# Kernel tuning notes

Hardware: AMD Instinct MI355X
Metric: run time of the kernel (lower is better)

## Reference

```python
import jax, jax.numpy as jnp
import numpy as np

B, H, W, ENC = 64, 14, 14, 2048
A, E, D, V, T = 512, 512, 512, 10000, 21


def setup_inputs() -> dict:
    key = jax.random.key(0)
    ks = jax.random.split(key, 24)
    f = lambda k, shape, s: (jax.random.normal(k, shape, jnp.float32) * s)
    inp = {
        'encoder_out': f(ks[0], (B, H, W, ENC), 1.0),
        'encoded_captions': jax.random.randint(ks[1], (B, T), 0, V),
        'caption_lengths': jax.random.randint(ks[2], (B,), 0, T + 1),
        'emb': jax.random.uniform(ks[3], (V, E), jnp.float32, -0.1, 0.1),
        'enc_att_W': f(ks[4], (ENC, A), 0.02), 'enc_att_b': jnp.zeros((A,), jnp.float32),
        'dec_att_W': f(ks[5], (D, A), 0.04), 'dec_att_b': jnp.zeros((A,), jnp.float32),
        'full_att_W': f(ks[6], (A, 1), 0.04), 'full_att_b': jnp.zeros((1,), jnp.float32),
        'init_h_W': f(ks[7], (ENC, D), 0.02), 'init_h_b': jnp.zeros((D,), jnp.float32),
        'init_c_W': f(ks[8], (ENC, D), 0.02), 'init_c_b': jnp.zeros((D,), jnp.float32),
        'f_beta_W': f(ks[9], (D, ENC), 0.04), 'f_beta_b': jnp.zeros((ENC,), jnp.float32),
        'W_ih': f(ks[10], (4 * D, E + ENC), 0.02), 'b_ih': jnp.zeros((4 * D,), jnp.float32),
        'W_hh': f(ks[11], (4 * D, D), 0.04), 'b_hh': jnp.zeros((4 * D,), jnp.float32),
        'fc_W': jax.random.uniform(ks[12], (D, V), jnp.float32, -0.1, 0.1),
        'fc_b': jnp.zeros((V,), jnp.float32),
    }
    return inp


def reference(encoder_out, encoded_captions, caption_lengths, emb,
              enc_att_W, enc_att_b, dec_att_W, dec_att_b, full_att_W, full_att_b,
              init_h_W, init_h_b, init_c_W, init_c_b, f_beta_W, f_beta_b,
              W_ih, b_ih, W_hh, b_hh, fc_W, fc_b):
    b = encoder_out.shape[0]
    enc = encoder_out.reshape(b, -1, encoder_out.shape[-1])  # (B, P, ENC)
    cl = jnp.clip(caption_lengths.reshape(-1), 1, None)
    sort_ind = jnp.argsort(-cl)  # descending by length
    cl = cl[sort_ind]
    enc = enc[sort_ind]
    caps = encoded_captions[sort_ind]
    dec_len = cl - 1  # (B,)

    embs = emb[caps]  # (B, T, E)
    mean_enc = enc.mean(axis=1)
    h0 = jnp.tanh(mean_enc @ init_h_W + init_h_b)
    c0 = jnp.tanh(mean_enc @ init_c_W + init_c_b)

    att1 = enc @ enc_att_W + enc_att_b  # (B, P, A), loop-invariant
    Tdec = caps.shape[1] - 1
    embs_t = jnp.swapaxes(embs[:, :Tdec], 0, 1)  # (Tdec, B, E)

    def step(carry, xs):
        h, c = carry
        t, x_emb = xs
        active = (t < dec_len)[:, None]  # (B,1)
        att2 = h @ dec_att_W + dec_att_b  # (B, A)
        e = jnp.squeeze(jax.nn.relu(att1 + att2[:, None, :]) @ full_att_W, -1) + full_att_b[0]  # (B,P)
        alpha = jax.nn.softmax(e + 1e-8, axis=1)
        awe = jnp.einsum('bpe,bp->be', enc, alpha)  # (B, ENC)
        gate = jax.nn.sigmoid(h @ f_beta_W + f_beta_b)
        awe = gate * awe
        x = jnp.concatenate([x_emb, awe], axis=1)  # (B, E+ENC)
        gates = x @ W_ih.T + b_ih + h @ W_hh.T + b_hh  # (B, 4D)
        i, f, g, o = jnp.split(gates, 4, axis=1)
        c_new = jax.nn.sigmoid(f) * c + jax.nn.sigmoid(i) * jnp.tanh(g)
        h_new = jax.nn.sigmoid(o) * jnp.tanh(c_new)
        preds = h_new @ fc_W + fc_b
        h = jnp.where(active, h_new, h)
        c = jnp.where(active, c_new, c)
        preds = jnp.where(active, preds, 0.0)
        alpha = jnp.where(active, alpha, 0.0)
        return (h, c), (preds, alpha)

    (_, _), (preds, alphas) = jax.lax.scan(step, (h0, c0), (jnp.arange(Tdec), embs_t))
    predictions = jnp.swapaxes(preds, 0, 1)  # (B, Tdec, V)
    alphas = jnp.swapaxes(alphas, 0, 1)      # (B, Tdec, P)
    return predictions, caps, dec_len, alphas, sort_ind
```

## Files before the change

### kernel.cpp

```cpp
#include <hip/hip_runtime.h>
#include <cstddef>


namespace {

typedef _Float16 f16;
typedef f16 f16x8 __attribute__((ext_vector_type(8)));
typedef f16 f16x4 __attribute__((ext_vector_type(4)));
typedef f16 f16x2 __attribute__((ext_vector_type(2)));
typedef float f32x4 __attribute__((ext_vector_type(4)));

constexpr int NB = 64, NP = 196, NE = 2048, NA = 512, ND = 512, NV = 10000;
constexpr int NT_CAP = 21, NTD = 20;
constexpr int KC = 3072;
constexpr int LDT = 40;
constexpr int LDK = 72;

constexpr size_t OFF_ATT1   = 0;
constexpr size_t OFF_DAW    = 12845056;
constexpr size_t OFF_FBW    = 13369344;
constexpr size_t OFF_EAW    = 15466496;
constexpr size_t OFF_IHW    = 17563648;
constexpr size_t OFF_ICW    = 19660800;
constexpr size_t OFF_FCW    = 15466496;
constexpr size_t OFF_WCAT   = 25755648;
constexpr size_t OFF_MEAN16 = 38338560;
constexpr size_t OFF_H16    = 38600704;
constexpr size_t OFF_HNEW16 = 38666240;
constexpr size_t OFF_C      = 38731776;
constexpr size_t OFF_ATT2   = 38862848;
constexpr size_t OFF_GATE   = 38993920;
constexpr size_t OFF_ALPHA  = 39518208;
constexpr size_t OFF_XCAT   = 39569408;
constexpr size_t OFF_INT    = 39962624;
constexpr size_t OFF_BCAT   = 39970816;
constexpr size_t OFF_ENC16  = 39979008;
constexpr size_t FULL_BYTES = 91359232;
constexpr size_t OFF_HSEQ   = FULL_BYTES;
constexpr size_t FULL2_BYTES = FULL_BYTES + (size_t)NTD * NB * ND * 2;
constexpr size_t OFF_HWHH   = FULL2_BYTES;
constexpr size_t OFF_EMBW   = OFF_HWHH + 524288;
constexpr size_t OFF_EMBS   = OFF_EMBW + 10485760;
constexpr size_t FULL3_BYTES = OFF_EMBS + 1310720;

__device__ __forceinline__ float sigmoidf_(float x) { return 1.0f / (1.0f + expf(-x)); }

__device__ __forceinline__ void stage16(const f16* __restrict__ src, int lda, int k0,
                                        f16* __restrict__ lds, int tid) {
  const int row = tid >> 2, seg = tid & 3;
  *(f16x8*)&lds[row * LDT + seg * 8] =
      *(const f16x8*)&src[(size_t)row * lda + k0 + seg * 8];
}

__device__ __forceinline__ void cvt8(const float* __restrict__ p, f16* __restrict__ dst) {
  const float4 a = *(const float4*)p;
// ... 295 lines not shown
                                                 f16* __restrict__ att1) {
  __shared__ __align__(16) f16 lA[64 * LDK];
  __shared__ __align__(16) f16 lB[128 * LDK];
  const int r0 = blockIdx.x * 64, n0 = blockIdx.y * 128;
  const int tid = threadIdx.x, lane = tid & 63, wv = tid >> 6;
  const int col = lane & 15, quad = lane >> 4;
  const int wr = wv >> 1, wc = wv & 1;
  const int arow = tid >> 2, aseg = (tid & 3) * 16;
  const int brow = tid >> 1, bseg = (tid & 1) * 32;
  const f16* gA = enc16 + (size_t)(r0 + arow) * NE + aseg;
  const f16* gB = eaWt + (size_t)(n0 + brow) * NE + bseg;
  f16* wA = &lA[arow * LDK + aseg];
  f16* wB = &lB[brow * LDK + bseg];
  f32x4 acc[2][4] = {};
  for (int k0 = 0; k0 < NE; k0 += 64) {
    *(f16x8*)(wA)      = *(const f16x8*)(gA + k0);
    *(f16x8*)(wA + 8)  = *(const f16x8*)(gA + k0 + 8);
    *(f16x8*)(wB)      = *(const f16x8*)(gB + k0);
    *(f16x8*)(wB + 8)  = *(const f16x8*)(gB + k0 + 8);
    *(f16x8*)(wB + 16) = *(const f16x8*)(gB + k0 + 16);
    *(f16x8*)(wB + 24) = *(const f16x8*)(gB + k0 + 24);
    __syncthreads();
#pragma unroll
    for (int kh = 0; kh < 2; ++kh) {
      f16x8 a[2], b[4];
#pragma unroll
      for (int i = 0; i < 2; ++i)
        a[i] = *(const f16x8*)&lA[(wr * 32 + i * 16 + col) * LDK + kh * 32 + quad * 8];
#pragma unroll
      for (int j = 0; j < 4; ++j)
        b[j] = *(const f16x8*)&lB[(wc * 64 + j * 16 + col) * LDK + kh * 32 + quad * 8];
#pragma unroll
      for (int i = 0; i < 2; ++i)
#pragma unroll
        for (int j = 0; j < 4; ++j)
          acc[i][j] = __builtin_amdgcn_mfma_f32_16x16x32_f16(a[i], b[j], acc[i][j], 0, 0, 0);
    }
    __syncthreads();
  }
#pragma unroll
  for (int j = 0; j < 4; ++j) {
    const int n = n0 + wc * 64 + j * 16 + col;
    const float bv = eab[n];
#pragma unroll
    for (int i = 0; i < 2; ++i)
#pragma unroll
      for (int rr = 0; rr < 4; ++rr) {
        const int r = r0 + wr * 32 + i * 16 + quad * 4 + rr;
        att1[(size_t)r * NA + n] = (f16)(acc[i][j][rr] + bv);
      }
  }
}

__global__ __launch_bounds__(256) void k_hgemm_v2(const f16* __restrict__ h16,
                                                  const f16* __restrict__ daWt,
                                                  const float* __restrict__ dab,
                                                  const f16* __restrict__ fbWt,
                                                  const float* __restrict__ fbb,
                                                  float* __restrict__ att2,
                                                  float* __restrict__ gate) {
  __shared__ float R[2 * 64 * 16];
  const int tid = threadIdx.x, lane = tid & 63, wv = tid >> 6;
  const int col = lane & 15, quad = lane >> 4;
  const int sub = wv >> 1, kh = wv & 1;
  const int nt = blockIdx.x * 2 + sub;
  const bool is_att = nt < 32;
  const f16* Brow = is_att ? (daWt + (size_t)nt * 16 * ND)
                           : (fbWt + (size_t)(nt - 32) * 16 * ND);
  f32x4 acc[4] = {};
  wave_gemm64(h16, Brow, ND, kh * 256, kh * 256 + 256, col, quad, acc);
  if (kh) {
#pragma unroll
    for (int mt = 0; mt < 4; ++mt)
#pragma unroll
      for (int rr = 0; rr < 4; ++rr)
        R[(sub * 64 + lane) * 16 + mt * 4 + rr] = acc[mt][rr];
  }
  __syncthreads();
  if (kh) return;
#pragma unroll
  for (int mt = 0; mt < 4; ++mt)
#pragma unroll
    for (int rr = 0; rr < 4; ++rr)
      acc[mt][rr] += R[(sub * 64 + lane) * 16 + mt * 4 + rr];
  if (is_att) {
    const int n = nt * 16 + col;
#pragma unroll
    for (int mt = 0; mt < 4; ++mt)
#pragma unroll
      for (int rr = 0; rr < 4; ++rr) {
        const int m = mt * 16 + quad * 4 + rr;
        att2[(size_t)m * NA + n] = acc[mt][rr] + dab[n];
      }
  } else {
    const int n = (nt - 32) * 16 + col;
#pragma unroll
    for (int mt = 0; mt < 4; ++mt)
#pragma unroll
      for (int rr = 0; rr < 4; ++rr) {
        const int m = mt * 16 + quad * 4 + rr;
        gate[(size_t)m * NE + n] = sigmoidf_(acc[mt][rr] + fbb[n]);
      }
  }
}

__global__ __launch_bounds__(256) void k_hall(const f16* __restrict__ h16,
                                              const f16* __restrict__ daWt,
                                              const float* __restrict__ dab,
                                              const f16* __restrict__ fbWt,
                                              const float* __restrict__ fbb,
                                              const f16* __restrict__ Wcat2,
                                              float* __restrict__ att2,
                                              float* __restrict__ gate,
                                              float* __restrict__ hwhh) {
  __shared__ float R[4 * 1024];
  const int nt = blockIdx.x;
  const int tid = threadIdx.x, lane = tid & 63, wv = tid >> 6;
  const int col = lane & 15, quad = lane >> 4;
  const f16* Brow; int ldb;
  if (nt < 32)       { Brow = daWt + (size_t)nt * 16 * ND; ldb = ND; }
  else if (nt < 160) { Brow = fbWt + (size_t)(nt - 32) * 16 * ND; ldb = ND; }
  else               { Brow = Wcat2 + (size_t)(nt - 160) * 16 * KC + 2560; ldb = KC; }
  f32x4 acc[4] = {};
  wave_gemm_s<4>(h16, ND, Brow, ldb, wv * 128, wv * 128 + 128, col, quad, acc);
#pragma unroll
  for (int mt = 0; mt < 4; ++mt)
#pragma unroll
    for (int rr = 0; rr < 4; ++rr)
      R[wv * 1024 + (mt * 4 + rr) * 64 + lane] = acc[mt][rr];
  __syncthreads();
#pragma unroll
  for (int j = 0; j < 4; ++j) {
    const int slot = tid * 4 + j;
    const float s = R[slot] + R[1024 + slot] + R[2048 + slot] + R[3072 + slot];
    const int c2 = slot >> 6;
    const int lane_s = slot & 63;
    const int mt = c2 >> 2, rr = c2 & 3;
    const int m = mt * 16 + (lane_s >> 4) * 4 + rr;
    const int nl = lane_s & 15;
    if (nt < 32) {
      const int n = nt * 16 + nl;
      att2[(size_t)m * NA + n] = s + dab[n];
    } else if (nt < 160) {
      const int n = (nt - 32) * 16 + nl;
      gate[(size_t)m * NE + n] = sigmoidf_(s + fbb[n]);
    } else {
      const int r = (nt - 160) * 16 + nl;
      hwhh[(size_t)m * NE + r] = s;
    }
  }
}

__global__ __launch_bounds__(512) void k_logits(const f16* __restrict__ att1,
                                                const float* __restrict__ att2,
                                                const float* __restrict__ fullW,
                                                const int* __restrict__ declen, int t,
                                                float* __restrict__ alpha_ws,
                                                float* __restrict__ out_alphas) {
  const int b = blockIdx.x;
  const int tid = threadIdx.x, wv = tid >> 6, lane = tid & 63;
  __shared__ float e[200];
  __shared__ float red2[2];
  {
    float a2r[8], fwr[8];
    const float4* A2 = (const float4*)(att2 + (size_t)b * NA + lane * 8);
    const float4* FW = (const float4*)(fullW + lane * 8);
    const float4 q0 = A2[0], q1 = A2[1], w0 = FW[0], w1 = FW[1];
    a2r[0] = q0.x; a2r[1] = q0.y; a2r[2] = q0.z; a2r[3] = q0.w;
    a2r[4] = q1.x; a2r[5] = q1.y; a2r[6] = q1.z; a2r[7] = q1.w;
    fwr[0] = w0.x; fwr[1] = w0.y; fwr[2] = w0.z; fwr[3] = w0.w;
    fwr[4] = w1.x; fwr[5] = w1.y; fwr[6] = w1.z; fwr[7] = w1.w;
    for (int p = wv; p < NP; p += 8) {
      const f16x8 row = *(const f16x8*)(att1 + ((size_t)b * NP + p) * NA + lane * 8);
      float acc = 0.0f;
#pragma unroll
      for (int j = 0; j < 8; ++j) acc += fmaxf((float)row[j] + a2r[j], 0.0f) * fwr[j];
#pragma unroll
      for (int off = 32; off > 0; off >>= 1) acc += __shfl_down(acc, off, 64);
      if (lane == 0) e[p] = acc;
    }
  }
  __syncthreads();
  if (wv == 0) {
    const float v0 = e[lane];
    const float v1 = e[lane + 64];
    const float v2 = e[lane + 128];
    const float v3 = (lane < 4) ? e[192 + lane] : -INFINITY;
    float mx = fmaxf(fmaxf(v0, v1), fmaxf(v2, v3));
#pragma unroll
    for (int off = 32; off > 0; off >>= 1) mx = fmaxf(mx, __shfl_xor(mx, off, 64));
    float s = expf(v0 - mx) + expf(v1 - mx) + expf(v2 - mx) +
              ((lane < 4) ? expf(v3 - mx) : 0.0f);
#pragma unroll
    for (int off = 32; off > 0; off >>= 1) s += __shfl_xor(s, off, 64);
    if (lane == 0) { red2[0] = mx; red2[1] = 1.0f / s; }
  }
  __syncthreads();
  if (tid < NP) {
    const float a = expf(e[tid] - red2[0]) * red2[1];
    alpha_ws[(size_t)b * NP + tid] = a;
    const bool act = t < declen[b];
    out_alphas[((size_t)b * NTD + t) * NP + tid] = act ? a : 0.0f;
  }
}

__global__ __launch_bounds__(256) void k_awe(const f16* __restrict__ enc16,
                                             const float* __restrict__ alpha_ws,
                                             const float* __restrict__ gate,
                                             f16* __restrict__ xcat) {
  const int b = blockIdx.x >> 2, q = blockIdx.x & 3;
  const int tid = threadIdx.x;
  __shared__ float al[NP];
  if (tid < NP) al[tid] = alpha_ws[(size_t)b * NP + tid];
  __syncthreads();
  const int c = q * 512 + tid * 2;
  const f16* base = enc16 + (size_t)b * NP * NE + c;
  float a0 = 0.0f, a1 = 0.0f, b0 = 0.0f, b1 = 0.0f;
  for (int p = 0; p < NP; p += 2) {
    const f16x2 v0 = *(const f16x2*)&base[(size_t)p * NE];
    const f16x2 v1 = *(const f16x2*)&base[(size_t)(p + 1) * NE];
    const float ap0 = al[p], ap1 = al[p + 1];
    a0 += ap0 * (float)v0[0]; a1 += ap0 * (float)v0[1];
    b0 += ap1 * (float)v1[0]; b1 += ap1 * (float)v1[1];
  }
  a0 += b0; a1 += b1;
  const float2 g = *(const float2*)&gate[(size_t)b * NE + c];
  f16x2 o; o[0] = (f16)(a0 * g.x); o[1] = (f16)(a1 * g.y);
  *(f16x2*)&xcat[(size_t)b * KC + 512 + c] = o;
}

template <bool E16>
__global__ __launch_bounds__(512) void k_attn_awe(const f16* __restrict__ att1,
                                                  const float* __restrict__ att2,
                                                  const float* __restrict__ fullW,
                                                  const int* __restrict__ declen, int t,
                                                  const float* __restrict__ encf,
                                                  const f16* __restrict__ enc16,
                                                  const int* __restrict__ perm,
                                                  const float* __restrict__ gate,
                                                  const float* __restrict__ emb,
                                                  const int* __restrict__ caps_s,
                                                  const f16* __restrict__ h16,
                                                  f16* __restrict__ xcat,
                                                  float* __restrict__ out_alphas) {
  const int b = blockIdx.x;
  const int tid = threadIdx.x, wv = tid >> 6, lane = tid & 63;
  __shared__ float e[200];
  __shared__ float al[200];
  __shared__ float red2[2];
  {
    float a2r[8], fwr[8];
    const float4* A2 = (const float4*)(att2 + (size_t)b * NA + lane * 8);
    const float4* FW = (const float4*)(fullW + lane * 8);
    const float4 q0 = A2[0], q1 = A2[1], w0 = FW[0], w1 = FW[1];
    a2r[0] = q0.x; a2r[1] = q0.y; a2r[2] = q0.z; a2r[3] = q0.w;
    a2r[4] = q1.x; a2r[5] = q1.y; a2r[6] = q1.z; a2r[7] = q1.w;
    fwr[0] = w0.x; fwr[1] = w0.y; fwr[2] = w0.z; fwr[3] = w0.w;
    fwr[4] = w1.x; fwr[5] = w1.y; fwr[6] = w1.z; fwr[7] = w1.w;
    for (int p = wv; p < NP; p += 8) {
      const f16x8 row = *(const f16x8*)(att1 + ((size_t)b * NP + p) * NA + lane * 8);
      float acc = 0.0f;
#pragma unroll
      for (int j = 0; j < 8; ++j) acc += fmaxf((float)row[j] + a2r[j], 0.0f) * fwr[j];
#pragma unroll
      for (int off = 32; off > 0; off >>= 1) acc += __shfl_down(acc, off, 64);
      if (lane == 0) e[p] = acc;
    }
  }
  __syncthreads();
  if (wv == 0) {
    const float v0 = e[lane];
    const float v1 = e[lane + 64];
    const float v2 = e[lane + 128];
    const float v3 = (lane < 4) ? e[192 + lane] : -INFINITY;
    float mx = fmaxf(fmaxf(v0, v1), fmaxf(v2, v3));
#pragma unroll
    for (int off = 32; off > 0; off >>= 1) mx = fmaxf(mx, __shfl_xor(mx, off, 64));
    float s = expf(v0 - mx) + expf(v1 - mx) + expf(v2 - mx) +
              ((lane < 4) ? expf(v3 - mx) : 0.0f);
#pragma unroll
    for (int off = 32; off > 0; off >>= 1) s += __shfl_xor(s, off, 64);
// ... 54 lines not shown
                                                  f16* __restrict__ hnew16,
                                                  f16* __restrict__ hseq) {
  __shared__ float R[8 * 64 * 16];
  const int nt = blockIdx.x;
  const int tid = threadIdx.x, lane = tid & 63, wv = tid >> 6;
  const int col = lane & 15, quad = lane >> 4;
  f32x4 acc[4] = {};
  wave_gemm64(xcat, Wcat2 + (size_t)nt * 16 * KC, KC, wv * 384, wv * 384 + 384,
              col, quad, acc);
#pragma unroll
  for (int mt = 0; mt < 4; ++mt)
#pragma unroll
    for (int rr = 0; rr < 4; ++rr)
      R[(wv * 64 + lane) * 16 + mt * 4 + rr] = acc[mt][rr];
  __syncthreads();
  {
    const int j0 = tid * 2;
#pragma unroll
    for (int j = 0; j < 2; ++j) {
      const int e2 = j0 + j;
      float s = R[e2];
#pragma unroll
      for (int w = 1; w < 8; ++w) s += R[w * 1024 + e2];
      R[e2] = s;
    }
  }
  __syncthreads();
  if (tid < 256) {
    const int m = tid >> 2, dl = tid & 3;
    const int mt = m >> 4, qd = (m >> 2) & 3, rr = m & 3;
    float g4[4];
#pragma unroll
    for (int g = 0; g < 4; ++g) {
      const int cv = dl * 4 + g;
      g4[g] = R[(qd * 16 + cv) * 16 + mt * 4 + rr] + bcat[nt * 16 + cv];
    }
    const int d = nt * 4 + dl;
    const float iv = sigmoidf_(g4[0]);
    const float fv = sigmoidf_(g4[1]);
    const float gv = tanhf(g4[2]);
    const float ov = sigmoidf_(g4[3]);
    const float cold = cst[(size_t)m * ND + d];
    const float cn = fv * cold + iv * gv;
    const float hn = ov * tanhf(cn);
    hnew16[(size_t)m * ND + d] = (f16)hn;
    if (hseq) hseq[((size_t)t * NB + m) * ND + d] = (f16)hn;
    if (t < declen[m]) {
      cst[(size_t)m * ND + d] = cn;
      h16[(size_t)m * ND + d] = (f16)hn;
    }
  }
}

__global__ __launch_bounds__(512) void k_xlstm_v3(const f16* __restrict__ xcat,
                                                  const f16* __restrict__ Wcat2,
                                                  const float* __restrict__ bcat,
                                                  const float* __restrict__ hwhh,
                                                  const float* __restrict__ embw,
                                                  const int* __restrict__ declen, int t,
                                                  float* __restrict__ cst,
                                                  f16* __restrict__ h16,
                                                  f16* __restrict__ hnew16,
                                                  f16* __restrict__ hseq) {
  __shared__ float R[8 * 512];
  const int nt = blockIdx.x >> 1, mh = blockIdx.x & 1;
  const int tid = threadIdx.x, lane = tid & 63, wv = tid >> 6;
  const int col = lane & 15, quad = lane >> 4;
  f32x4 acc[2] = {};
  wave_gemm_s<2>(xcat + (size_t)mh * 32 * KC, KC,
                 Wcat2 + (size_t)nt * 16 * KC, KC,
                 512 + wv * 256, 512 + wv * 256 + 256, col, quad, acc);
#pragma unroll
  for (int mt = 0; mt < 2; ++mt)
#pragma unroll
    for (int rr = 0; rr < 4; ++rr)
      R[wv * 512 + (mt * 4 + rr) * 64 + lane] = acc[mt][rr];
  __syncthreads();
  {
    float s = R[tid];
#pragma unroll
    for (int w = 1; w < 8; ++w) s += R[w * 512 + tid];
    R[tid] = s;
  }
  __syncthreads();
  if (tid < 128) {
    const int ml = tid >> 2, dl = tid & 3;
    const int m = mh * 32 + ml;
    const int d = nt * 4 + dl;
    const int mt = ml >> 4, qd = (ml >> 2) & 3, rr = ml & 3;
    float g4[4];
#pragma unroll
    for (int g = 0; g < 4; ++g) {
      const int cv = dl * 4 + g;
      const int r = nt * 16 + cv;
      const float s = R[(mt * 4 + rr) * 64 + qd * 16 + cv];
      g4[g] = s + bcat[r] + hwhh[(size_t)m * NE + r] +
              embw[((size_t)t * NB + m) * NE + r];
    }
    const float iv = sigmoidf_(g4[0]);
    const float fv = sigmoidf_(g4[1]);
    const float gv = tanhf(g4[2]);
    const float ov = sigmoidf_(g4[3]);
    const float cold = cst[(size_t)m * ND + d];
    const float cn = fv * cold + iv * gv;
    const float hn = ov * tanhf(cn);
    hnew16[(size_t)m * ND + d] = (f16)hn;
    hseq[((size_t)t * NB + m) * ND + d] = (f16)hn;
    if (t < declen[m]) {
      cst[(size_t)m * ND + d] = cn;
      h16[(size_t)m * ND + d] = (f16)hn;
    }
  }
}

__global__ __launch_bounds__(256) void k_fc_mfma(const f16* __restrict__ hnew16,
                                                 const f16* __restrict__ fcWt,
                                                 const float* __restrict__ fcb,
                                                 const int* __restrict__ declen, int t,
                                                 float* __restrict__ out_pred) {
  const int tid = threadIdx.x, lane = tid & 63, wv = tid >> 6;
  const int col = lane & 15, quad = lane >> 4;
  const int nt = blockIdx.x * 4 + wv;
  f32x4 acc[4] = {};
  wave_gemm64(hnew16, fcWt + (size_t)nt * 16 * ND, ND, 0, ND, col, quad, acc);
  const int n = nt * 16 + col;
  if (n < NV) {
    const float bv = fcb[n];
#pragma unroll
    for (int mt = 0; mt < 4; ++mt)
#pragma unroll
      for (int rr = 0; rr < 4; ++rr) {
        const int m = mt * 16 + quad * 4 + rr;
        const bool act = t < declen[m];
        out_pred[((size_t)m * NTD + t) * NV + n] = act ? (acc[mt][rr] + bv) : 0.0f;
      }
  }
}

__global__ __launch_bounds__(256) void k_fc_v2(const f16* __restrict__ hseq,
                                               const f16* __restrict__ fcWt,
                                               const float* __restrict__ fcb,
                                               const int* __restrict__ declen,
                                               float* __restrict__ out_pred) {
  __shared__ __align__(16) f16 lA[256 * LDK];
  __shared__ __align__(16) f16 lB[64 * LDK];
  const int n0 = blockIdx.x * 64, m0 = blockIdx.y * 256;
  const int tid = threadIdx.x, lane = tid & 63, wv = tid >> 6;
  const int col = lane & 15, quad = lane >> 4;
  const f16* gA = hseq + (size_t)(m0 + tid) * ND;
  const f16* gB = fcWt + (size_t)(n0 + (tid >> 2)) * ND + (tid & 3) * 16;
  f16* wA = &lA[tid * LDK];
  f16* wB = &lB[(tid >> 2) * LDK + (tid & 3) * 16];
  f32x4 acc[4][4] = {};
  for (int k0 = 0; k0 < ND; k0 += 64) {
#pragma unroll
    for (int u = 0; u < 8; ++u)
      *(f16x8*)(wA + u * 8) = *(const f16x8*)(gA + k0 + u * 8);
    *(f16x8*)(wB)     = *(const f16x8*)(gB + k0);
    *(f16x8*)(wB + 8) = *(const f16x8*)(gB + k0 + 8);
    __syncthreads();
#pragma unroll
    for (int kh = 0; kh < 2; ++kh) {
      f16x8 a[4], b[4];
#pragma unroll
      for (int i = 0; i < 4; ++i)
        a[i] = *(const f16x8*)&lA[(wv * 64 + i * 16 + col) * LDK + kh * 32 + quad * 8];
#pragma unroll
      for (int j = 0; j < 4; ++j)
        b[j] = *(const f16x8*)&lB[(j * 16 + col) * LDK + kh * 32 + quad * 8];
#pragma unroll
      for (int i = 0; i < 4; ++i)
#pragma unroll
        for (int j = 0; j < 4; ++j)
          acc[i][j] = __builtin_amdgcn_mfma_f32_16x16x32_f16(a[i], b[j], acc[i][j], 0, 0, 0);
    }
    __syncthreads();
  }
#pragma unroll
  for (int j = 0; j < 4; ++j) {
    const int n = n0 + j * 16 + col;
    if (n >= NV) continue;
    const float bv = fcb[n];
#pragma unroll
    for (int i = 0; i < 4; ++i)
#pragma unroll
      for (int rr = 0; rr < 4; ++rr) {
        const int r = m0 + wv * 64 + i * 16 + quad * 4 + rr;
        const int tt = r >> 6, m = r & 63;
        const bool act = tt < declen[m];
        out_pred[((size_t)m * NTD + tt) * NV + n] = act ? (acc[i][j][rr] + bv) : 0.0f;
      }
  }
}

}

extern "C" void kernel_launch(void* const* d_in, const int* in_sizes, int n_in,
                              void* d_out, int out_size, void* d_ws, size_t ws_size,
                              hipStream_t stream) {
  const float* enc        = (const float*)d_in[0];
  const int*   caps       = (const int*)d_in[1];
  const int*   caplen     = (const int*)d_in[2];
  const float* emb        = (const float*)d_in[3];
  const float* enc_att_W  = (const float*)d_in[4];
  const float* enc_att_b  = (const float*)d_in[5];
  const float* dec_att_W  = (const float*)d_in[6];
  const float* dec_att_b  = (const float*)d_in[7];
  const float* full_att_W = (const float*)d_in[8];
  const float* init_h_W   = (const float*)d_in[10];
  const float* init_h_b   = (const float*)d_in[11];
  const float* init_c_W   = (const float*)d_in[12];
  const float* init_c_b   = (const float*)d_in[13];
  const float* f_beta_W   = (const float*)d_in[14];
  const float* f_beta_b   = (const float*)d_in[15];
  const float* W_ih       = (const float*)d_in[16];
  const float* b_ih       = (const float*)d_in[17];
  const float* W_hh       = (const float*)d_in[18];
  const float* b_hh       = (const float*)d_in[19];
  const float* fc_W       = (const float*)d_in[20];
  const float* fc_b       = (const float*)d_in[21];

  char* ws = (char*)d_ws;
  f16*   att1   = (f16*)(ws + OFF_ATT1);
  f16*   daWt   = (f16*)(ws + OFF_DAW);
  f16*   fbWt   = (f16*)(ws + OFF_FBW);
  f16*   eaWt   = (f16*)(ws + OFF_EAW);
  f16*   ihWt   = (f16*)(ws + OFF_IHW);
  f16*   icWt   = (f16*)(ws + OFF_ICW);
  f16*   fcWt   = (f16*)(ws + OFF_FCW);
  f16*   Wcat2  = (f16*)(ws + OFF_WCAT);
  f16*   mean16 = (f16*)(ws + OFF_MEAN16);
  f16*   h16    = (f16*)(ws + OFF_H16);
  f16*   hnew16 = (f16*)(ws + OFF_HNEW16);
  float* cst    = (float*)(ws + OFF_C);
  float* att2   = (float*)(ws + OFF_ATT2);
  float* gate   = (float*)(ws + OFF_GATE);
  float* alpha  = (float*)(ws + OFF_ALPHA);
  f16*   xcat   = (f16*)(ws + OFF_XCAT);
  int*   wsi    = (int*)(ws + OFF_INT);
  int*   perm   = wsi;
  int*   declen = wsi + 64;
  int*   caps_s = wsi + 128;
  float* bcat   = (float*)(ws + OFF_BCAT);
  f16*   enc16  = (f16*)(ws + OFF_ENC16);
  float* hwhh   = (float*)(ws + OFF_HWHH);
  float* embw   = (float*)(ws + OFF_EMBW);
  f16*   embs16 = (f16*)(ws + OFF_EMBS);

  const bool full  = ws_size >= FULL_BYTES;
  const bool batch = ws_size >= FULL2_BYTES;
  const bool full3 = ws_size >= FULL3_BYTES;
  f16* hseq = batch ? (f16*)(ws + OFF_HSEQ) : (f16*)nullptr;

  float* out         = (float*)d_out;
  float* out_pred    = out;
  float* out_caps    = out_pred + (size_t)NB * NTD * NV;
  float* out_declen  = out_caps + (size_t)NB * NT_CAP;
  float* out_alphas  = out_declen + NB;
  float* out_sortind = out_alphas + (size_t)NB * NTD * NP;

  k_sort<<<1, 64, 0, stream>>>(caplen, caps, perm, declen, caps_s,
                               out_caps, out_declen, out_sortind);
  k_tconv<<<dim3(16, 64), 256, 0, stream>>>(enc_att_W, eaWt, 2048, 512);
  k_tconv<<<dim3(16, 16), 256, 0, stream>>>(dec_att_W, daWt, 512, 512);
  k_tconv<<<dim3(64, 16), 256, 0, stream>>>(f_beta_W, fbWt, 512, 2048);
  k_tconv<<<dim3(16, 64), 256, 0, stream>>>(init_h_W, ihWt, 2048, 512);
  k_tconv<<<dim3(16, 64), 256, 0, stream>>>(init_c_W, icWt, 2048, 512);
  if (full) {
    k_enc_cvt<<<dim3(196, 64), 256, 0, stream>>>(enc, perm, enc16);
    k_mean16<<<dim3(4, 64), 256, 0, stream>>>(enc16, mean16);
  } else {
    k_mean<<<dim3(4, 64), 256, 0, stream>>>(enc, perm, mean16);
  }
  k_init_mfma<<<dim3(16, 2), 256, 0, stream>>>(mean16, ihWt, icWt, init_h_b, init_c_b,
                                               h16, cst);
  if (full)
    k_att1_v2<<<dim3(196, 4), 256, 0, stream>>>(enc16, eaWt, enc_att_b, att1);
  else
    k_att1_mfma<false><<<dim3(4, 196), 256, 0, stream>>>(enc, enc16, perm, eaWt,
                                                         enc_att_b, att1);
  k_tconv<<<dim3(314, 16), 256, 0, stream>>>(fc_W, fcWt, 512, NV);
  k_cvt_wcat2<<<2048, 256, 0, stream>>>(W_ih, W_hh, b_ih, b_hh, Wcat2, bcat);
  if (full3) {
    k_embs<<<dim3(NTD, NB), 256, 0, stream>>>(emb, caps_s, embs16);
    k_embw<<<dim3(32, 5), 256, 0, stream>>>(embs16, Wcat2, embw);
  }

  if (full3) {
    for (int t = 0; t < NTD; ++t) {
      k_hall<<<288, 256, 0, stream>>>(h16, daWt, dec_att_b, fbWt, f_beta_b, Wcat2,
                                      att2, gate, hwhh);
      k_logits<<<NB, 512, 0, stream>>>(att1, att2, full_att_W, declen, t,
                                       alpha, out_alphas);
      k_awe<<<256, 256, 0, stream>>>(enc16, alpha, gate, xcat);
      k_xlstm_v3<<<256, 512, 0, stream>>>(xcat, Wcat2, bcat, hwhh, embw, declen, t,
                                          cst, h16, hnew16, hseq);
    }
    k_fc_v2<<<dim3(157, 5), 256, 0, stream>>>(hseq, fcWt, fc_b, declen, out_pred);
  } else {
    for (int t = 0; t < NTD; ++t) {
      k_hgemm_v2<<<80, 256, 0, stream>>>(h16, daWt, dec_att_b, fbWt, f_beta_b,
                                         att2, gate);
      if (full)
        k_attn_awe<true><<<NB, 512, 0, stream>>>(att1, att2, full_att_W, declen, t,
                                                 enc, enc16, perm, gate, emb, caps_s,
                                                 h16, xcat, out_alphas);
      else
        k_attn_awe<false><<<NB, 512, 0, stream>>>(att1, att2, full_att_W, declen, t,
                                                  enc, enc16, perm, gate, emb, caps_s,
                                                  h16, xcat, out_alphas);
      k_xlstm_v2<<<128, 512, 0, stream>>>(xcat, Wcat2, bcat, declen, t,
                                          cst, h16, hnew16, hseq);
      if (!batch)
        k_fc_mfma<<<157, 256, 0, stream>>>(hnew16, fcWt, fc_b, declen, t, out_pred);
    }
    if (batch)
      k_fc_v2<<<dim3(157, 5), 256, 0, stream>>>(hseq, fcWt, fc_b, declen, out_pred);
  }
}
```

Measured before the change: 1.304 ms.

## Fuse per-timestep decoder kernels into one persistent cooperative kernel with grid syncs

Replaces the 80 per-step launches (hall, logits, awe, xlstm over 20 timesteps) with a single cooperative persistent kernel. Grid-wide syncs separate the phases, and blocks loop over tiles in grid-stride fashion. This removes kernel launch overhead and gaps between launches. In exchange the grid is capped by occupancy (up to 256 blocks of 512 threads), so some phases get less parallelism than before, and grid.sync adds its own cost. The old kernels were moved in the file and remain as a fallback path.

```diff
diff --git a/kernel.cpp b/kernel.cpp
--- a/kernel.cpp
+++ b/kernel.cpp
@@ -1,6 +1,9 @@
 #include <hip/hip_runtime.h>
+#include <hip/hip_cooperative_groups.h>
 #include <cstddef>
 
+
+namespace cg = cooperative_groups;
 
 namespace {
 
@@ -402,6 +405,199 @@
   }
 }
 
+struct StepParams {
+  f16* h16;
+  const f16* daWt; const float* dab;
+  const f16* fbWt; const float* fbb;
+  const f16* Wcat2; const float* bcat;
+  const f16* att1; const float* fullW;
+  const f16* enc16;
+  const float* embw;
+  const int* declen;
+  float* att2; float* gate; float* hwhh;
+  float* alpha; float* out_alphas;
+  f16* xcat;
+  float* cst;
+  f16* hseq;
+};
+
+__global__ __launch_bounds__(512, 2) void k_steps(StepParams P) {
+  cg::grid_group grid = cg::this_grid();
+  __shared__ float S[8192];
+  const int tid = threadIdx.x, lane = tid & 63, wv = tid >> 6;
+  const int col = lane & 15, quad = lane >> 4;
+  const int bid = blockIdx.x, nblk = gridDim.x;
+
+  for (int t = 0; t < NTD; ++t) {
+    for (int nt = bid; nt < 288; nt += nblk) {
+      const f16* Brow; int ldb;
+      if (nt < 32)       { Brow = P.daWt + (size_t)nt * 16 * ND; ldb = ND; }
+      else if (nt < 160) { Brow = P.fbWt + (size_t)(nt - 32) * 16 * ND; ldb = ND; }
+      else               { Brow = P.Wcat2 + (size_t)(nt - 160) * 16 * KC + 2560; ldb = KC; }
+      f32x4 acc[4] = {};
+      wave_gemm_s<4>(P.h16, ND, Brow, ldb, wv * 64, wv * 64 + 64, col, quad, acc);
+#pragma unroll
+      for (int mt = 0; mt < 4; ++mt)
+#pragma unroll
+        for (int rr = 0; rr < 4; ++rr)
+          S[wv * 1024 + (mt * 4 + rr) * 64 + lane] = acc[mt][rr];
+      __syncthreads();
+#pragma unroll
+      for (int j = 0; j < 2; ++j) {
+        const int slot = tid * 2 + j;
+        float s = S[slot];
+#pragma unroll
+        for (int w = 1; w < 8; ++w) s += S[w * 1024 + slot];
+        const int c2 = slot >> 6, lane_s = slot & 63;
+        const int mt = c2 >> 2, rr = c2 & 3;
+        const int m = mt * 16 + (lane_s >> 4) * 4 + rr;
+        const int nl = lane_s & 15;
+        if (nt < 32) {
+          const int n = nt * 16 + nl;
+          P.att2[(size_t)m * NA + n] = s + P.dab[n];
+        } else if (nt < 160) {
+          const int n = (nt - 32) * 16 + nl;
+          P.gate[(size_t)m * NE + n] = sigmoidf_(s + P.fbb[n]);
+        } else {
+          const int r = (nt - 160) * 16 + nl;
+          P.hwhh[(size_t)m * NE + r] = s;
+        }
+      }
+      __syncthreads();
+    }
+    __threadfence();
+    grid.sync();
+
+    for (int b = bid; b < NB; b += nblk) {
+      float a2r[8], fwr[8];
+      {
+        const float4* A2 = (const float4*)(P.att2 + (size_t)b * NA + lane * 8);
+        const float4* FW = (const float4*)(P.fullW + lane * 8);
+        const float4 q0 = A2[0], q1 = A2[1], w0 = FW[0], w1 = FW[1];
+        a2r[0] = q0.x; a2r[1] = q0.y; a2r[2] = q0.z; a2r[3] = q0.w;
+        a2r[4] = q1.x; a2r[5] = q1.y; a2r[6] = q1.z; a2r[7] = q1.w;
+        fwr[0] = w0.x; fwr[1] = w0.y; fwr[2] = w0.z; fwr[3] = w0.w;
+        fwr[4] = w1.x; fwr[5] = w1.y; fwr[6] = w1.z; fwr[7] = w1.w;
+      }
+      for (int p = wv; p < NP; p += 8) {
+        const f16x8 row = *(const f16x8*)(P.att1 + ((size_t)b * NP + p) * NA + lane * 8);
+        float acc = 0.0f;
+#pragma unroll
+        for (int j = 0; j < 8; ++j) acc += fmaxf((float)row[j] + a2r[j], 0.0f) * fwr[j];
+#pragma unroll
+        for (int off = 32; off > 0; off >>= 1) acc += __shfl_down(acc, off, 64);
+        if (lane == 0) S[p] = acc;
+      }
+      __syncthreads();
+      if (wv == 0) {
+        const float v0 = S[lane];
+        const float v1 = S[lane + 64];
+        const float v2 = S[lane + 128];
+        const float v3 = (lane < 4) ? S[192 + lane] : -INFINITY;
+        float mx = fmaxf(fmaxf(v0, v1), fmaxf(v2, v3));
+#pragma unroll
+        for (int off = 32; off > 0; off >>= 1) mx = fmaxf(mx, __shfl_xor(mx, off, 64));
+        float s = expf(v0 - mx) + expf(v1 - mx) + expf(v2 - mx) +
+                  ((lane < 4) ? expf(v3 - mx) : 0.0f);
+#pragma unroll
+        for (int off = 32; off > 0; off >>= 1) s += __shfl_xor(s, off, 64);
+        if (lane == 0) { S[200] = mx; S[201] = 1.0f / s; }
+      }
+      __syncthreads();
+      if (tid < NP) {
+        const float a = expf(S[tid] - S[200]) * S[201];
+        P.alpha[(size_t)b * NP + tid] = a;
+        const bool act = t < P.declen[b];
+        P.out_alphas[((size_t)b * NTD + t) * NP + tid] = act ? a : 0.0f;
+      }
+      __syncthreads();
+    }
+    __threadfence();
+    grid.sync();
+
+    for (int task = bid; task < 256; task += nblk) {
+      const int b = task >> 2, q = task & 3;
+      if (tid < NP) S[tid] = P.alpha[(size_t)b * NP + tid];
+      __syncthreads();
+      const int cl = (tid & 255) * 2, ph = tid >> 8;
+      const int c = q * 512 + cl;
+      const f16* base = P.enc16 + (size_t)b * NP * NE + c;
+      float a0 = 0.0f, a1 = 0.0f;
+      const int p0 = ph ? 98 : 0, p1 = ph ? 196 : 98;
+      for (int p = p0; p < p1; ++p) {
+        const f16x2 v = *(const f16x2*)&base[(size_t)p * NE];
+        const float ap = S[p];
+        a0 += ap * (float)v[0]; a1 += ap * (float)v[1];
+      }
+      S[256 + ph * 512 + cl] = a0;
+      S[256 + ph * 512 + cl + 1] = a1;
+      __syncthreads();
+      if (tid < 256) {
+        const int c2 = tid * 2;
+        const float r0 = S[256 + c2] + S[768 + c2];
+        const float r1 = S[256 + c2 + 1] + S[768 + c2 + 1];
+        const int cc = q * 512 + c2;
+        const float2 g = *(const float2*)&P.gate[(size_t)b * NE + cc];
+        f16x2 o; o[0] = (f16)(r0 * g.x); o[1] = (f16)(r1 * g.y);
+        *(f16x2*)&P.xcat[(size_t)b * KC + 512 + cc] = o;
+      }
+      __syncthreads();
+    }
+    __threadfence();
+    grid.sync();
+
+    for (int task = bid; task < 256; task += nblk) {
+      const int nt = task >> 1, mh = task & 1;
+      f32x4 acc[2] = {};
+      wave_gemm_s<2>(P.xcat + (size_t)mh * 32 * KC, KC,
+                     P.Wcat2 + (size_t)nt * 16 * KC, KC,
+                     512 + wv * 256, 512 + wv * 256 + 256, col, quad, acc);
+#pragma unroll
+      for (int mt = 0; mt < 2; ++mt)
+#pragma unroll
+        for (int rr = 0; rr < 4; ++rr)
+          S[wv * 512 + (mt * 4 + rr) * 64 + lane] = acc[mt][rr];
+      __syncthreads();
+      {
+        float s = S[tid];
+#pragma unroll
+        for (int w = 1; w < 8; ++w) s += S[w * 512 + tid];
+        S[tid] = s;
+      }
+      __syncthreads();
+      if (tid < 128) {
+        const int ml = tid >> 2, dl = tid & 3;
+        const int m = mh * 32 + ml;
+        const int d = nt * 4 + dl;
+        const int mt = ml >> 4, qd = (ml >> 2) & 3, rr = ml & 3;
+        float g4[4];
+#pragma unroll
+        for (int g = 0; g < 4; ++g) {
+          const int cv = dl * 4 + g;
+          const int r = nt * 16 + cv;
+          g4[g] = S[(mt * 4 + rr) * 64 + qd * 16 + cv] + P.bcat[r] +
+                  P.hwhh[(size_t)m * NE + r] + P.embw[((size_t)t * NB + m) * NE + r];
+        }
+        const float iv = sigmoidf_(g4[0]);
+        const float fv = sigmoidf_(g4[1]);
+        const float gv = tanhf(g4[2]);
+        const float ov = sigmoidf_(g4[3]);
+        const float cold = P.cst[(size_t)m * ND + d];
+        const float cn = fv * cold + iv * gv;
+        const float hn = ov * tanhf(cn);
+        P.hseq[((size_t)t * NB + m) * ND + d] = (f16)hn;
+        if (t < P.declen[m]) {
+          P.cst[(size_t)m * ND + d] = cn;
+          P.h16[(size_t)m * ND + d] = (f16)hn;
+        }
+      }
+      __syncthreads();
+    }
+    __threadfence();
+    grid.sync();
+  }
+}
+
 __global__ __launch_bounds__(256) void k_hgemm_v2(const f16* __restrict__ h16,
                                                   const f16* __restrict__ daWt,
                                                   const float* __restrict__ dab,
@@ -452,131 +648,6 @@
         gate[(size_t)m * NE + n] = sigmoidf_(acc[mt][rr] + fbb[n]);
       }
   }
-}
-
-__global__ __launch_bounds__(256) void k_hall(const f16* __restrict__ h16,
-                                              const f16* __restrict__ daWt,
-                                              const float* __restrict__ dab,
-                                              const f16* __restrict__ fbWt,
-                                              const float* __restrict__ fbb,
-                                              const f16* __restrict__ Wcat2,
-                                              float* __restrict__ att2,
-                                              float* __restrict__ gate,
-                                              float* __restrict__ hwhh) {
-  __shared__ float R[4 * 1024];
-  const int nt = blockIdx.x;
-  const int tid = threadIdx.x, lane = tid & 63, wv = tid >> 6;
-  const int col = lane & 15, quad = lane >> 4;
-  const f16* Brow; int ldb;
-  if (nt < 32)       { Brow = daWt + (size_t)nt * 16 * ND; ldb = ND; }
-  else if (nt < 160) { Brow = fbWt + (size_t)(nt - 32) * 16 * ND; ldb = ND; }
-  else               { Brow = Wcat2 + (size_t)(nt - 160) * 16 * KC + 2560; ldb = KC; }
-  f32x4 acc[4] = {};
-  wave_gemm_s<4>(h16, ND, Brow, ldb, wv * 128, wv * 128 + 128, col, quad, acc);
-#pragma unroll
-  for (int mt = 0; mt < 4; ++mt)
-#pragma unroll
-    for (int rr = 0; rr < 4; ++rr)
-      R[wv * 1024 + (mt * 4 + rr) * 64 + lane] = acc[mt][rr];
-  __syncthreads();
-#pragma unroll
-  for (int j = 0; j < 4; ++j) {
-    const int slot = tid * 4 + j;
-    const float s = R[slot] + R[1024 + slot] + R[2048 + slot] + R[3072 + slot];
-    const int c2 = slot >> 6;
-    const int lane_s = slot & 63;
-    const int mt = c2 >> 2, rr = c2 & 3;
-    const int m = mt * 16 + (lane_s >> 4) * 4 + rr;
-    const int nl = lane_s & 15;
-    if (nt < 32) {
-      const int n = nt * 16 + nl;
-      att2[(size_t)m * NA + n] = s + dab[n];
-    } else if (nt < 160) {
-      const int n = (nt - 32) * 16 + nl;
-      gate[(size_t)m * NE + n] = sigmoidf_(s + fbb[n]);
-    } else {
-      const int r = (nt - 160) * 16 + nl;
-      hwhh[(size_t)m * NE + r] = s;
-    }
-  }
-}
-
-__global__ __launch_bounds__(512) void k_logits(const f16* __restrict__ att1,
-                                                const float* __restrict__ att2,
-                                                const float* __restrict__ fullW,
-                                                const int* __restrict__ declen, int t,
-                                                float* __restrict__ alpha_ws,
-                                                float* __restrict__ out_alphas) {
-  const int b = blockIdx.x;
-  const int tid = threadIdx.x, wv = tid >> 6, lane = tid & 63;
-  __shared__ float e[200];
-  __shared__ float red2[2];
-  {
-    float a2r[8], fwr[8];
-    const float4* A2 = (const float4*)(att2 + (size_t)b * NA + lane * 8);
-    const float4* FW = (const float4*)(fullW + lane * 8);
-    const float4 q0 = A2[0], q1 = A2[1], w0 = FW[0], w1 = FW[1];
-    a2r[0] = q0.x; a2r[1] = q0.y; a2r[2] = q0.z; a2r[3] = q0.w;
-    a2r[4] = q1.x; a2r[5] = q1.y; a2r[6] = q1.z; a2r[7] = q1.w;
-    fwr[0] = w0.x; fwr[1] = w0.y; fwr[2] = w0.z; fwr[3] = w0.w;
-    fwr[4] = w1.x; fwr[5] = w1.y; fwr[6] = w1.z; fwr[7] = w1.w;
-    for (int p = wv; p < NP; p += 8) {
-      const f16x8 row = *(const f16x8*)(att1 + ((size_t)b * NP + p) * NA + lane * 8);
-      float acc = 0.0f;
-#pragma unroll
-      for (int j = 0; j < 8; ++j) acc += fmaxf((float)row[j] + a2r[j], 0.0f) * fwr[j];
-#pragma unroll
-      for (int off = 32; off > 0; off >>= 1) acc += __shfl_down(acc, off, 64);
-      if (lane == 0) e[p] = acc;
-    }
-  }
-  __syncthreads();
-  if (wv == 0) {
-    const float v0 = e[lane];
-    const float v1 = e[lane + 64];
-    const float v2 = e[lane + 128];
-    const float v3 = (lane < 4) ? e[192 + lane] : -INFINITY;
-    float mx = fmaxf(fmaxf(v0, v1), fmaxf(v2, v3));
-#pragma unroll
-    for (int off = 32; off > 0; off >>= 1) mx = fmaxf(mx, __shfl_xor(mx, off, 64));
-    float s = expf(v0 - mx) + expf(v1 - mx) + expf(v2 - mx) +
-              ((lane < 4) ? expf(v3 - mx) : 0.0f);
-#pragma unroll
-    for (int off = 32; off > 0; off >>= 1) s += __shfl_xor(s, off, 64);
-    if (lane == 0) { red2[0] = mx; red2[1] = 1.0f / s; }
-  }
-  __syncthreads();
-  if (tid < NP) {
-    const float a = expf(e[tid] - red2[0]) * red2[1];
-    alpha_ws[(size_t)b * NP + tid] = a;
-    const bool act = t < declen[b];
-    out_alphas[((size_t)b * NTD + t) * NP + tid] = act ? a : 0.0f;
-  }
-}
-
-__global__ __launch_bounds__(256) void k_awe(const f16* __restrict__ enc16,
-                                             const float* __restrict__ alpha_ws,
-                                             const float* __restrict__ gate,
-                                             f16* __restrict__ xcat) {
-  const int b = blockIdx.x >> 2, q = blockIdx.x & 3;
-  const int tid = threadIdx.x;
-  __shared__ float al[NP];
-  if (tid < NP) al[tid] = alpha_ws[(size_t)b * NP + tid];
-  __syncthreads();
-  const int c = q * 512 + tid * 2;
-  const f16* base = enc16 + (size_t)b * NP * NE + c;
-  float a0 = 0.0f, a1 = 0.0f, b0 = 0.0f, b1 = 0.0f;
-  for (int p = 0; p < NP; p += 2) {
-    const f16x2 v0 = *(const f16x2*)&base[(size_t)p * NE];
-    const f16x2 v1 = *(const f16x2*)&base[(size_t)(p + 1) * NE];
-    const float ap0 = al[p], ap1 = al[p + 1];
-    a0 += ap0 * (float)v0[0]; a1 += ap0 * (float)v0[1];
-    b0 += ap1 * (float)v1[0]; b1 += ap1 * (float)v1[1];
-  }
-  a0 += b0; a1 += b1;
-  const float2 g = *(const float2*)&gate[(size_t)b * NE + c];
-  f16x2 o; o[0] = (f16)(a0 * g.x); o[1] = (f16)(a1 * g.y);
-  *(f16x2*)&xcat[(size_t)b * KC + 512 + c] = o;
 }
 
 template <bool E16>
@@ -737,6 +808,211 @@
   }
 }
 
+__global__ __launch_bounds__(256) void k_fc_mfma(const f16* __restrict__ hnew16,
+                                                 const f16* __restrict__ fcWt,
+                                                 const float* __restrict__ fcb,
+                                                 const int* __restrict__ declen, int t,
+                                                 float* __restrict__ out_pred) {
+  const int tid = threadIdx.x, lane = tid & 63, wv = tid >> 6;
+  const int col = lane & 15, quad = lane >> 4;
+  const int nt = blockIdx.x * 4 + wv;
+  f32x4 acc[4] = {};
+  wave_gemm64(hnew16, fcWt + (size_t)nt * 16 * ND, ND, 0, ND, col, quad, acc);
+  const int n = nt * 16 + col;
+  if (n < NV) {
+    const float bv = fcb[n];
+#pragma unroll
+    for (int mt = 0; mt < 4; ++mt)
+#pragma unroll
+      for (int rr = 0; rr < 4; ++rr) {
+        const int m = mt * 16 + quad * 4 + rr;
+        const bool act = t < declen[m];
+        out_pred[((size_t)m * NTD + t) * NV + n] = act ? (acc[mt][rr] + bv) : 0.0f;
+      }
+  }
+}
+
+__global__ __launch_bounds__(256) void k_fc_v2(const f16* __restrict__ hseq,
+                                               const f16* __restrict__ fcWt,
+                                               const float* __restrict__ fcb,
+                                               const int* __restrict__ declen,
+                                               float* __restrict__ out_pred) {
+  __shared__ __align__(16) f16 lA[256 * LDK];
+  __shared__ __align__(16) f16 lB[64 * LDK];
+  const int n0 = blockIdx.x * 64, m0 = blockIdx.y * 256;
+  const int tid = threadIdx.x, lane = tid & 63, wv = tid >> 6;
+  const int col = lane & 15, quad = lane >> 4;
+  const f16* gA = hseq + (size_t)(m0 + tid) * ND;
+  const f16* gB = fcWt + (size_t)(n0 + (tid >> 2)) * ND + (tid & 3) * 16;
+  f16* wA = &lA[tid * LDK];
+  f16* wB = &lB[(tid >> 2) * LDK + (tid & 3) * 16];
+  f32x4 acc[4][4] = {};
+  for (int k0 = 0; k0 < ND; k0 += 64) {
+#pragma unroll
+    for (int u = 0; u < 8; ++u)
+      *(f16x8*)(wA + u * 8) = *(const f16x8*)(gA + k0 + u * 8);
+    *(f16x8*)(wB)     = *(const f16x8*)(gB + k0);
+    *(f16x8*)(wB + 8) = *(const f16x8*)(gB + k0 + 8);
+    __syncthreads();
+#pragma unroll
+    for (int kh = 0; kh < 2; ++kh) {
+      f16x8 a[4], b[4];
+#pragma unroll
+      for (int i = 0; i < 4; ++i)
+        a[i] = *(const f16x8*)&lA[(wv * 64 + i * 16 + col) * LDK + kh * 32 + quad * 8];
+#pragma unroll
+      for (int j = 0; j < 4; ++j)
+        b[j] = *(const f16x8*)&lB[(j * 16 + col) * LDK + kh * 32 + quad * 8];
+#pragma unroll
+      for (int i = 0; i < 4; ++i)
+#pragma unroll
+        for (int j = 0; j < 4; ++j)
+          acc[i][j] = __builtin_amdgcn_mfma_f32_16x16x32_f16(a[i], b[j], acc[i][j], 0, 0, 0);
+    }
+    __syncthreads();
+  }
+#pragma unroll
+  for (int j = 0; j < 4; ++j) {
+    const int n = n0 + j * 16 + col;
+    if (n >= NV) continue;
+    const float bv = fcb[n];
+#pragma unroll
+    for (int i = 0; i < 4; ++i)
+#pragma unroll
+      for (int rr = 0; rr < 4; ++rr) {
+        const int r = m0 + wv * 64 + i * 16 + quad * 4 + rr;
+        const int tt = r >> 6, m = r & 63;
+        const bool act = tt < declen[m];
+        out_pred[((size_t)m * NTD + tt) * NV + n] = act ? (acc[i][j][rr] + bv) : 0.0f;
+      }
+  }
+}
+
+__global__ __launch_bounds__(256) void k_hall(const f16* __restrict__ h16,
+                                              const f16* __restrict__ daWt,
+                                              const float* __restrict__ dab,
+                                              const f16* __restrict__ fbWt,
+                                              const float* __restrict__ fbb,
+                                              const f16* __restrict__ Wcat2,
+                                              float* __restrict__ att2,
+                                              float* __restrict__ gate,
+                                              float* __restrict__ hwhh) {
+  __shared__ float R[4 * 1024];
+  const int nt = blockIdx.x;
+  const int tid = threadIdx.x, lane = tid & 63, wv = tid >> 6;
+  const int col = lane & 15, quad = lane >> 4;
+  const f16* Brow; int ldb;
+  if (nt < 32)       { Brow = daWt + (size_t)nt * 16 * ND; ldb = ND; }
+  else if (nt < 160) { Brow = fbWt + (size_t)(nt - 32) * 16 * ND; ldb = ND; }
+  else               { Brow = Wcat2 + (size_t)(nt - 160) * 16 * KC + 2560; ldb = KC; }
+  f32x4 acc[4] = {};
+  wave_gemm_s<4>(h16, ND, Brow, ldb, wv * 128, wv * 128 + 128, col, quad, acc);
+#pragma unroll
+  for (int mt = 0; mt < 4; ++mt)
+#pragma unroll
+    for (int rr = 0; rr < 4; ++rr)
+      R[wv * 1024 + (mt * 4 + rr) * 64 + lane] = acc[mt][rr];
+  __syncthreads();
+#pragma unroll
+  for (int j = 0; j < 4; ++j) {
+    const int slot = tid * 4 + j;
+    const float s = R[slot] + R[1024 + slot] + R[2048 + slot] + R[3072 + slot];
+    const int c2 = slot >> 6;
+    const int lane_s = slot & 63;
+    const int mt = c2 >> 2, rr = c2 & 3;
+    const int m = mt * 16 + (lane_s >> 4) * 4 + rr;
+    const int nl = lane_s & 15;
+    if (nt < 32) {
+      const int n = nt * 16 + nl;
+      att2[(size_t)m * NA + n] = s + dab[n];
+    } else if (nt < 160) {
+      const int n = (nt - 32) * 16 + nl;
+      gate[(size_t)m * NE + n] = sigmoidf_(s + fbb[n]);
+    } else {
+      const int r = (nt - 160) * 16 + nl;
+      hwhh[(size_t)m * NE + r] = s;
+    }
+  }
+}
+
+__global__ __launch_bounds__(512) void k_logits(const f16* __restrict__ att1,
+                                                const float* __restrict__ att2,
+                                                const float* __restrict__ fullW,
+                                                const int* __restrict__ declen, int t,
+                                                float* __restrict__ alpha_ws,
+                                                float* __restrict__ out_alphas) {
+  const int b = blockIdx.x;
+  const int tid = threadIdx.x, wv = tid >> 6, lane = tid & 63;
+  __shared__ float e[200];
+  __shared__ float red2[2];
+  {
+    float a2r[8], fwr[8];
+    const float4* A2 = (const float4*)(att2 + (size_t)b * NA + lane * 8);
+    const float4* FW = (const float4*)(fullW + lane * 8);
+    const float4 q0 = A2[0], q1 = A2[1], w0 = FW[0], w1 = FW[1];
+    a2r[0] = q0.x; a2r[1] = q0.y; a2r[2] = q0.z; a2r[3] = q0.w;
+    a2r[4] = q1.x; a2r[5] = q1.y; a2r[6] = q1.z; a2r[7] = q1.w;
+    fwr[0] = w0.x; fwr[1] = w0.y; fwr[2] = w0.z; fwr[3] = w0.w;
+    fwr[4] = w1.x; fwr[5] = w1.y; fwr[6] = w1.z; fwr[7] = w1.w;
+    for (int p = wv; p < NP; p += 8) {
+      const f16x8 row = *(const f16x8*)(att1 + ((size_t)b * NP + p) * NA + lane * 8);
+      float acc = 0.0f;
+#pragma unroll
+      for (int j = 0; j < 8; ++j) acc += fmaxf((float)row[j] + a2r[j], 0.0f) * fwr[j];
+#pragma unroll
+      for (int off = 32; off > 0; off >>= 1) acc += __shfl_down(acc, off, 64);
+      if (lane == 0) e[p] = acc;
+    }
+  }
+  __syncthreads();
+  if (wv == 0) {
+    const float v0 = e[lane];
+    const float v1 = e[lane + 64];
+    const float v2 = e[lane + 128];
+    const float v3 = (lane < 4) ? e[192 + lane] : -INFINITY;
+    float mx = fmaxf(fmaxf(v0, v1), fmaxf(v2, v3));
+#pragma unroll
+    for (int off = 32; off > 0; off >>= 1) mx = fmaxf(mx, __shfl_xor(mx, off, 64));
+    float s = expf(v0 - mx) + expf(v1 - mx) + expf(v2 - mx) +
+              ((lane < 4) ? expf(v3 - mx) : 0.0f);
+#pragma unroll
+    for (int off = 32; off > 0; off >>= 1) s += __shfl_xor(s, off, 64);
+    if (lane == 0) { red2[0] = mx; red2[1] = 1.0f / s; }
+  }
+  __syncthreads();
+  if (tid < NP) {
+    const float a = expf(e[tid] - red2[0]) * red2[1];
+    alpha_ws[(size_t)b * NP + tid] = a;
+    const bool act = t < declen[b];
+    out_alphas[((size_t)b * NTD + t) * NP + tid] = act ? a : 0.0f;
+  }
+}
+
+__global__ __launch_bounds__(256) void k_awe(const f16* __restrict__ enc16,
+                                             const float* __restrict__ alpha_ws,
+                                             const float* __restrict__ gate,
+                                             f16* __restrict__ xcat) {
+  const int b = blockIdx.x >> 2, q = blockIdx.x & 3;
+  const int tid = threadIdx.x;
+  __shared__ float al[NP];
+  if (tid < NP) al[tid] = alpha_ws[(size_t)b * NP + tid];
+  __syncthreads();
+  const int c = q * 512 + tid * 2;
+  const f16* base = enc16 + (size_t)b * NP * NE + c;
+  float a0 = 0.0f, a1 = 0.0f, b0 = 0.0f, b1 = 0.0f;
+  for (int p = 0; p < NP; p += 2) {
+    const f16x2 v0 = *(const f16x2*)&base[(size_t)p * NE];
+    const f16x2 v1 = *(const f16x2*)&base[(size_t)(p + 1) * NE];
+    const float ap0 = al[p], ap1 = al[p + 1];
+    a0 += ap0 * (float)v0[0]; a1 += ap0 * (float)v0[1];
+    b0 += ap1 * (float)v1[0]; b1 += ap1 * (float)v1[1];
+  }
+  a0 += b0; a1 += b1;
+  const float2 g = *(const float2*)&gate[(size_t)b * NE + c];
+  f16x2 o; o[0] = (f16)(a0 * g.x); o[1] = (f16)(a1 * g.y);
+  *(f16x2*)&xcat[(size_t)b * KC + 512 + c] = o;
+}
+
 __global__ __launch_bounds__(512) void k_xlstm_v3(const f16* __restrict__ xcat,
                                                   const f16* __restrict__ Wcat2,
                                                   const float* __restrict__ bcat,
@@ -795,86 +1071,6 @@
       cst[(size_t)m * ND + d] = cn;
       h16[(size_t)m * ND + d] = (f16)hn;
     }
-  }
-}
-
-__global__ __launch_bounds__(256) void k_fc_mfma(const f16* __restrict__ hnew16,
-                                                 const f16* __restrict__ fcWt,
-                                                 const float* __restrict__ fcb,
-                                                 const int* __restrict__ declen, int t,
-                                                 float* __restrict__ out_pred) {
-  const int tid = threadIdx.x, lane = tid & 63, wv = tid >> 6;
-  const int col = lane & 15, quad = lane >> 4;
-  const int nt = blockIdx.x * 4 + wv;
-  f32x4 acc[4] = {};
-  wave_gemm64(hnew16, fcWt + (size_t)nt * 16 * ND, ND, 0, ND, col, quad, acc);
-  const int n = nt * 16 + col;
-  if (n < NV) {
-    const float bv = fcb[n];
-#pragma unroll
-    for (int mt = 0; mt < 4; ++mt)
-#pragma unroll
-      for (int rr = 0; rr < 4; ++rr) {
-        const int m = mt * 16 + quad * 4 + rr;
-        const bool act = t < declen[m];
-        out_pred[((size_t)m * NTD + t) * NV + n] = act ? (acc[mt][rr] + bv) : 0.0f;
-      }
-  }
-}
-
-__global__ __launch_bounds__(256) void k_fc_v2(const f16* __restrict__ hseq,
-                                               const f16* __restrict__ fcWt,
-                                               const float* __restrict__ fcb,
-                                               const int* __restrict__ declen,
-                                               float* __restrict__ out_pred) {
-  __shared__ __align__(16) f16 lA[256 * LDK];
-  __shared__ __align__(16) f16 lB[64 * LDK];
-  const int n0 = blockIdx.x * 64, m0 = blockIdx.y * 256;
-  const int tid = threadIdx.x, lane = tid & 63, wv = tid >> 6;
-  const int col = lane & 15, quad = lane >> 4;
-  const f16* gA = hseq + (size_t)(m0 + tid) * ND;
-  const f16* gB = fcWt + (size_t)(n0 + (tid >> 2)) * ND + (tid & 3) * 16;
-  f16* wA = &lA[tid * LDK];
-  f16* wB = &lB[(tid >> 2) * LDK + (tid & 3) * 16];
-  f32x4 acc[4][4] = {};
-  for (int k0 = 0; k0 < ND; k0 += 64) {
-#pragma unroll
-    for (int u = 0; u < 8; ++u)
-      *(f16x8*)(wA + u * 8) = *(const f16x8*)(gA + k0 + u * 8);
-    *(f16x8*)(wB)     = *(const f16x8*)(gB + k0);
-    *(f16x8*)(wB + 8) = *(const f16x8*)(gB + k0 + 8);
-    __syncthreads();
-#pragma unroll
-    for (int kh = 0; kh < 2; ++kh) {
-      f16x8 a[4], b[4];
-#pragma unroll
-      for (int i = 0; i < 4; ++i)
-        a[i] = *(const f16x8*)&lA[(wv * 64 + i * 16 + col) * LDK + kh * 32 + quad * 8];
-#pragma unroll
-      for (int j = 0; j < 4; ++j)
-        b[j] = *(const f16x8*)&lB[(j * 16 + col) * LDK + kh * 32 + quad * 8];
-#pragma unroll
-      for (int i = 0; i < 4; ++i)
-#pragma unroll
-        for (int j = 0; j < 4; ++j)
-          acc[i][j] = __builtin_amdgcn_mfma_f32_16x16x32_f16(a[i], b[j], acc[i][j], 0, 0, 0);
-    }
-    __syncthreads();
-  }
-#pragma unroll
-  for (int j = 0; j < 4; ++j) {
-    const int n = n0 + j * 16 + col;
-    if (n >= NV) continue;
-    const float bv = fcb[n];
-#pragma unroll
-    for (int i = 0; i < 4; ++i)
-#pragma unroll
-      for (int rr = 0; rr < 4; ++rr) {
-        const int r = m0 + wv * 64 + i * 16 + quad * 4 + rr;
-        const int tt = r >> 6, m = r & 63;
-        const bool act = tt < declen[m];
-        out_pred[((size_t)m * NTD + tt) * NV + n] = act ? (acc[i][j][rr] + bv) : 0.0f;
-      }
   }
 }
 
@@ -937,6 +1133,28 @@
   const bool full3 = ws_size >= FULL3_BYTES;
   f16* hseq = batch ? (f16*)(ws + OFF_HSEQ) : (f16*)nullptr;
 
+  bool coop_ok = false;
+  int coop_grid = 0;
+  if (full3) {
+    int dev = 0;
+    if (hipGetDevice(&dev) == hipSuccess) {
+      int coop = 0;
+      hipDeviceGetAttribute(&coop, hipDeviceAttributeCooperativeLaunch, dev);
+      if (coop) {
+        int ncu = 0;
+        hipDeviceGetAttribute(&ncu, hipDeviceAttributeMultiprocessorCount, dev);
+        int maxb = 0;
+        if (hipOccupancyMaxActiveBlocksPerMultiprocessor(
+                &maxb, reinterpret_cast<const void*>(&k_steps), 512, 0) == hipSuccess &&
+            maxb >= 1 && ncu > 0) {
+          coop_grid = maxb * ncu;
+          if (coop_grid > 256) coop_grid = 256;
+          coop_ok = coop_grid >= 64;
+        }
+      }
+    }
+  }
+
   float* out         = (float*)d_out;
   float* out_pred    = out;
   float* out_caps    = out_pred + (size_t)NB * NTD * NV;
@@ -971,7 +1189,18 @@
     k_embw<<<dim3(32, 5), 256, 0, stream>>>(embs16, Wcat2, embw);
   }
 
-  if (full3) {
+  if (full3 && coop_ok) {
+    StepParams P;
+    P.h16 = h16; P.daWt = daWt; P.dab = dec_att_b; P.fbWt = fbWt; P.fbb = f_beta_b;
+    P.Wcat2 = Wcat2; P.bcat = bcat; P.att1 = att1; P.fullW = full_att_W;
+    P.enc16 = enc16; P.embw = embw; P.declen = declen;
+    P.att2 = att2; P.gate = gate; P.hwhh = hwhh; P.alpha = alpha;
+    P.out_alphas = out_alphas; P.xcat = xcat; P.cst = cst; P.hseq = hseq;
+    void* args[] = { &P };
+    hipLaunchCooperativeKernel(reinterpret_cast<const void*>(&k_steps),
+                               dim3(coop_grid), dim3(512), args, 0, stream);
+    k_fc_v2<<<dim3(157, 5), 256, 0, stream>>>(hseq, fcWt, fc_b, declen, out_pred);
+  } else if (full3) {
     for (int t = 0; t < NTD; ++t) {
       k_hall<<<288, 256, 0, stream>>>(h16, daWt, dec_att_b, fbWt, f_beta_b, Wcat2,
                                       att2, gate, hwhh);
```

New measurement: 1.305 ms. About the same (+0.1%).
